# Optimization experiments

Measured on AMD Instinct MI355X. Metric: run time of the kernel, lower is better.

## Reference

```python
import jax, jax.numpy as jnp
import numpy as np

RES = 64
FDIM = 32
NMOD = 3
HID = 64
NCLS = 4
NFREQ = 6
IN_DIM = FDIM * NMOD + 3 * (2 * NFREQ + 1)  # 135


def trilinear_sample(grid, pts):
    """Torch F.grid_sample(mode='bilinear', padding_mode='zeros', align_corners=True).
    grid: [C, D, H, W]; pts: [M, 3] with (x, y, z) in [-1, 1], x indexes W, y->H, z->D.
    Returns [M, C]."""
    C, D, H, W = grid.shape
    x, y, z = pts[:, 0], pts[:, 1], pts[:, 2]
    ix = (x + 1.0) * 0.5 * (W - 1)
    iy = (y + 1.0) * 0.5 * (H - 1)
    iz = (z + 1.0) * 0.5 * (D - 1)
    ix0 = jnp.floor(ix); iy0 = jnp.floor(iy); iz0 = jnp.floor(iz)
    fx = ix - ix0; fy = iy - iy0; fz = iz - iz0
    ix0i = ix0.astype(jnp.int32); ix1i = ix0i + 1
    iy0i = iy0.astype(jnp.int32); iy1i = iy0i + 1
    iz0i = iz0.astype(jnp.int32); iz1i = iz0i + 1

    def corner(zc, yc, xc, w):
        valid = ((zc >= 0) & (zc < D) & (yc >= 0) & (yc < H) & (xc >= 0) & (xc < W))
        zcc = jnp.clip(zc, 0, D - 1)
        ycc = jnp.clip(yc, 0, H - 1)
        xcc = jnp.clip(xc, 0, W - 1)
        v = grid[:, zcc, ycc, xcc]  # [C, M]
        return v * (w * valid.astype(grid.dtype))

    wx0 = 1.0 - fx; wx1 = fx
    wy0 = 1.0 - fy; wy1 = fy
    wz0 = 1.0 - fz; wz1 = fz
    out = (corner(iz0i, iy0i, ix0i, wz0 * wy0 * wx0)
           + corner(iz0i, iy0i, ix1i, wz0 * wy0 * wx1)
           + corner(iz0i, iy1i, ix0i, wz0 * wy1 * wx0)
           + corner(iz0i, iy1i, ix1i, wz0 * wy1 * wx1)
           + corner(iz1i, iy0i, ix0i, wz1 * wy0 * wx0)
           + corner(iz1i, iy0i, ix1i, wz1 * wy0 * wx1)
           + corner(iz1i, iy1i, ix0i, wz1 * wy1 * wx0)
           + corner(iz1i, iy1i, ix1i, wz1 * wy1 * wx1))
    return out.T  # [M, C]


def positional_encoding(x):
    # gamma(p) = [p, sin(2^0 pi p), cos(2^0 pi p), ..., sin(2^(L-1) pi p), cos(2^(L-1) pi p)]
    freqs = 2.0 ** jnp.arange(NFREQ, dtype=x.dtype)  # [L]
    enc = [x]
    for i in range(NFREQ):
        a = jnp.pi * freqs[i] * x
        enc.append(jnp.sin(a))
        enc.append(jnp.cos(a))
    return jnp.concatenate(enc, axis=-1)  # [..., 3*(2L+1)]


def setup_inputs() -> dict:
    key = jax.random.key(0)
    ks = jax.random.split(key, 8)
    B, N = 4, 131072
    points = jax.random.uniform(ks[0], (B, N, 3), jnp.float32, -1.0, 1.0)
    grids = jax.random.normal(ks[1], (NMOD, FDIM, RES, RES, RES), jnp.float32) * 0.1

    def xavier(k, fan_in, fan_out):
        a = np.sqrt(6.0 / (fan_in + fan_out))
        return jax.random.uniform(k, (fan_in, fan_out), jnp.float32, -a, a)

    W0 = xavier(ks[2], IN_DIM, HID); b0 = jnp.zeros((HID,), jnp.float32)
    W1 = xavier(ks[3], HID, HID); b1 = jnp.zeros((HID,), jnp.float32)
    W2 = xavier(ks[4], HID, 1 + NCLS); b2 = jnp.zeros((1 + NCLS,), jnp.float32)
    return {"points": points, "grids": grids, "W0": W0, "b0": b0,
            "W1": W1, "b1": b1, "W2": W2, "b2": b2}


def reference(points, grids, W0, b0, W1, b1, W2, b2):
    B, N, _ = points.shape
    pts = points.reshape(B * N, 3)
    # fuse all 3 modalities: cat along feature dim, modality-major order
    feats = jax.vmap(lambda g: trilinear_sample(g, pts))(grids)  # [3, M, C]
    fused = jnp.transpose(feats, (1, 0, 2)).reshape(B * N, NMOD * FDIM)
    pe = positional_encoding(pts)  # [M, 39]
    h = jnp.concatenate([fused, pe], axis=-1)  # [M, 135]
    h = jax.nn.relu(h @ W0 + b0)
    h = jax.nn.relu(h @ W1 + b1)
    o = h @ W2 + b2  # [M, 1 + num_classes]
    density = jax.nn.softplus(o[..., 0]).reshape(B, N)
    seg_logits = o[..., 1:].reshape(B, N, NCLS)
    return density, seg_logits
```

## Files before the change

kernel.cpp:

```cpp
#include <hip/hip_runtime.h>
#include <hip/hip_bf16.h>
#include <hip/hip_fp16.h>
#include <math.h>

#define RESX 64
#define NVOX (RESX * RESX * RESX)
#define FDIM 32
#define NMOD 3
#define HID 64
#define NCLS 4
#define NFREQ 6
#define INDIM 135
#define TPB 64
#define XK 168
#define XSTR 65
#define MSTRIDE_B (NVOX * FDIM * 2)
#define NCELL 4096
#define NREP 16
#define TRB (NMOD * (NVOX / 64))
#define HISTB 2048
#define PACKB 15

typedef _Float16 f16x8 __attribute__((ext_vector_type(8)));
typedef float    f32x4 __attribute__((ext_vector_type(4)));

static __device__ __forceinline__ __half2 u2h(unsigned int u) {
    return __builtin_bit_cast(__half2, u);
}
static __device__ __forceinline__ unsigned int h2u(__half2 h) {
    return __builtin_bit_cast(unsigned int, h);
}

static __device__ __forceinline__ int cell_coords(float px, float py, float pz,
                                                  int& x0, int& y0, int& z0) {
    x0 = (int)floorf((px + 1.0f) * 0.5f * (RESX - 1));
    y0 = (int)floorf((py + 1.0f) * 0.5f * (RESX - 1));
    z0 = (int)floorf((pz + 1.0f) * 0.5f * (RESX - 1));
    x0 = min(max(x0, 0), RESX - 1);
    y0 = min(max(y0, 0), RESX - 1);
    z0 = min(max(z0, 0), RESX - 1);
    return ((z0 >> 2) << 8) | ((y0 >> 2) << 4) | (x0 >> 2);
}

#define W0PACK (5 * 4 * 64 * 8)
#define W1PACK (2 * 4 * 64 * 8)
#define W2PACK (2 * 64 * 8)

__global__ void pre_kernel(const float* __restrict__ g,
                           _Float16* __restrict__ gt,
                           const float* __restrict__ W0,
                           const float* __restrict__ W1,
                           const float* __restrict__ W2,
                           _Float16* __restrict__ wb,
                           const float* __restrict__ points,
                           unsigned int* __restrict__ hist, int M) {
    __shared__ float tile[FDIM][65];
    const int bid = blockIdx.x;
    const int t   = threadIdx.x;
    if (bid < TRB) {
        const int m  = bid >> 12;
        const int v0 = (bid & 4095) << 6;
#pragma unroll
        for (int pass = 0; pass < 8; ++pass) {
            const int c = pass * 4 + (t >> 6);
            const int v = t & 63;
            tile[c][v] = g[(size_t)(m * FDIM + c) * NVOX + v0 + v];
        }
        __syncthreads();
        unsigned int* gtu = reinterpret_cast<unsigned int*>(gt);
#pragma unroll
        for (int pass = 0; pass < 4; ++pass) {
            const int flat = pass * 256 + t;
            const int v  = flat >> 4;
            const int cu = flat & 15;
            gtu[(size_t)(m * NVOX + v0 + v) * 16 + cu] =
                h2u(__floats2half2_rn(tile[2 * cu][v], tile[2 * cu + 1][v]));
        }
    } else if (bid < TRB + HISTB) {
        const int hb = bid - TRB;
        const int i  = hb * 256 + t;
        const int r  = hb & (NREP - 1);
        if (i < M) {
            int x0, y0, z0;
            const int c = cell_coords(points[i * 3], points[i * 3 + 1], points[i * 3 + 2],
                                      x0, y0, z0);
            atomicAdd(&hist[r * NCELL + c], 1u);
        }
    } else {
        const int tt = (bid - TRB - HISTB) * 256 + t;
        const int NT = PACKB * 256;
        for (int idx = tt; idx < W0PACK; idx += NT) {
            const int j = idx & 7, l = (idx >> 3) & 63, nt = (idx >> 9) & 3, s = idx >> 11;
            const int k = 32 * s + (l >> 4) * 8 + j;
            const int o = 16 * nt + (l & 15);
            wb[idx] = (_Float16)((k < INDIM) ? W0[k * HID + o] : 0.0f);
        }
        for (int idx = tt; idx < W1PACK; idx += NT) {
            const int j = idx & 7, l = (idx >> 3) & 63, nt = (idx >> 9) & 3, s = idx >> 11;
            const int k = 32 * s + (l >> 4) * 8 + j;
            const int o = 16 * nt + (l & 15);
            wb[W0PACK + idx] = (_Float16)W1[k * HID + o];
        }
        for (int idx = tt; idx < W2PACK; idx += NT) {
            const int j = idx & 7, l = (idx >> 3) & 63, s = idx >> 9;
            const int k = 32 * s + (l >> 4) * 8 + j;
            const int o = l & 15;
            wb[W0PACK + W1PACK + idx] =
                (_Float16)((o < NCLS + 1) ? W2[k * (NCLS + 1) + o] : 0.0f);
        }
    }
}

__global__ __launch_bounds__(1024) void scan_fuse_kernel(unsigned int* __restrict__ hist) {
    __shared__ unsigned int s[1024];
    const int t = threadIdx.x;
    unsigned int tot[4];
#pragma unroll
    for (int j = 0; j < 4; ++j) {
        const int c = 4 * t + j;
        unsigned int run = 0;
#pragma unroll
        for (int r = 0; r < NREP; ++r) {
            const unsigned int v = hist[r * NCELL + c];
            hist[r * NCELL + c] = run;
            run += v;
        }
        tot[j] = run;
    }
    const unsigned int sum = tot[0] + tot[1] + tot[2] + tot[3];
    s[t] = sum;
    __syncthreads();
    for (int off = 1; off < 1024; off <<= 1) {
        const unsigned int x = (t >= off) ? s[t - off] : 0u;
        __syncthreads();
        s[t] += x;
        __syncthreads();
    }
    unsigned int cb = s[t] - sum;
#pragma unroll
    for (int j = 0; j < 4; ++j) {
        const int c = 4 * t + j;
#pragma unroll
        for (int r = 0; r < NREP; ++r) hist[r * NCELL + c] += cb;
        cb += tot[j];
    }
}

__global__ void scatter_kernel(const float* __restrict__ points,
                               unsigned int* __restrict__ hist,
                               float4* __restrict__ pts4, int M) {
    const int i = blockIdx.x * 256 + threadIdx.x;
    if (i < M) {
        const float px = points[i * 3], py = points[i * 3 + 1], pz = points[i * 3 + 2];
        int x0, y0, z0;
        const int c = cell_coords(px, py, pz, x0, y0, z0);
        const int r = blockIdx.x & (NREP - 1);
        const unsigned int pos = atomicAdd(&hist[r * NCELL + c], 1u);
        pts4[pos] = make_float4(px, py, pz, __int_as_float(i));
    }
}

template <bool SORT>
__global__ __launch_bounds__(256, 6) void fused_mfma_kernel(
    const float* __restrict__ points,
    const float4* __restrict__ pts4,
    const _Float16* __restrict__ gt,
    const _Float16* __restrict__ wb,
    const float* __restrict__ b0, const float* __restrict__ b1,
    const float* __restrict__ b2,
    float* __restrict__ density, float* __restrict__ seg) {
    __shared__ __align__(16) _Float16 Xs[TPB * XK];
    __shared__ __align__(16) int4   PB[TPB];
    __shared__ __align__(16) float4 PW[TPB];
    __shared__ __align__(16) float4 PXI[TPB];
    __shared__ int PIdx[TPB];
    const int tid = threadIdx.x;
    const int chunk = gridDim.x >> 3;
    const int sbid  = (blockIdx.x & 7) * chunk + (blockIdx.x >> 3);
    const int p0    = sbid * TPB;

    const int l = tid & 63;
    const int w = __builtin_amdgcn_readfirstlane(tid >> 6);

    if (l < 16) {
        const int p  = w * 16 + l;
        const int sp = p0 + p;
        float px, py, pz; int gp;
        if (SORT) {
            const float4 q = pts4[sp];
            px = q.x; py = q.y; pz = q.z; gp = __float_as_int(q.w);
        } else {
            px = points[sp * 3]; py = points[sp * 3 + 1]; pz = points[sp * 3 + 2];
            gp = sp;
        }
        const float ix = (px + 1.0f) * 0.5f * (RESX - 1);
        const float iy = (py + 1.0f) * 0.5f * (RESX - 1);
        const float iz = (pz + 1.0f) * 0.5f * (RESX - 1);
        const float fx0 = floorf(ix), fy0 = floorf(iy), fz0 = floorf(iz);
        const float fx = ix - fx0, fy = iy - fy0, fz = iz - fz0;
        int x0 = (int)fx0, y0 = (int)fy0, z0 = (int)fz0;
        x0 = min(max(x0, 0), RESX - 1);
        y0 = min(max(y0, 0), RESX - 1);
        z0 = min(max(z0, 0), RESX - 1);
        const int y1 = min(y0 + 1, RESX - 1);
        const int z1 = min(z0 + 1, RESX - 1);
        const float wy0 = 1.0f - fy, wy1 = fy;
        const float wz0 = 1.0f - fz, wz1 = fz;
        PB[p] = make_int4((z0 * 4096 + y0 * 64 + x0) * 64,
                          (z0 * 4096 + y1 * 64 + x0) * 64,
                          (z1 * 4096 + y0 * 64 + x0) * 64,
                          (z1 * 4096 + y1 * 64 + x0) * 64);
        PW[p]  = make_float4(wz0 * wy0, wz0 * wy1, wz1 * wy0, wz1 * wy1);
        PXI[p] = make_float4(px, py, pz, fx);
        PIdx[p] = gp;
    }

    {
        const int hw   = tid >> 5;
        const int lane = tid & 31;
        const int half = lane >> 4;
        const int lc   = lane & 15;
        const char* gbase = reinterpret_cast<const char*>(gt) + lane * 4;
#pragma unroll
        for (int i = 0; i < 8; ++i) {
            const int p = hw * 8 + i;
            const int4   bq = PB[p];
            const float4 wq = PW[p];
            const float  fx = PXI[p].w;
            const float wxh = half ? fx : 1.0f - fx;
            const __half2 h00 = __float2half2_rn(wq.x * wxh);
            const __half2 h01 = __float2half2_rn(wq.y * wxh);
            const __half2 h10 = __float2half2_rn(wq.z * wxh);
            const __half2 h11 = __float2half2_rn(wq.w * wxh);
            unsigned int accu[NMOD];
#pragma unroll
            for (int m = 0; m < NMOD; ++m) {
                const char* gm = gbase + (size_t)m * MSTRIDE_B;
                const unsigned int u0 = *reinterpret_cast<const unsigned int*>(gm + bq.x);
                const unsigned int u1 = *reinterpret_cast<const unsigned int*>(gm + bq.y);
                const unsigned int u2 = *reinterpret_cast<const unsigned int*>(gm + bq.z);
                const unsigned int u3 = *reinterpret_cast<const unsigned int*>(gm + bq.w);
                __half2 a = __hmul2(h00, u2h(u0));
                a = __hfma2(h01, u2h(u1), a);
                a = __hfma2(h10, u2h(u2), a);
                a = __hfma2(h11, u2h(u3), a);
                accu[m] = h2u(a);
            }
#pragma unroll
            for (int m = 0; m < NMOD; ++m) {
                const unsigned int other = __shfl_xor(accu[m], 16, 64);
                const __half2 sum = __hadd2(u2h(accu[m]), u2h(other));
                if (lane < 16) {
                    *reinterpret_cast<unsigned int*>(&Xs[p * XK + m * FDIM + 2 * lc]) = h2u(sum);
                }
            }
        }
    }

    {
        const int pt  = w * 16 + (l & 15);
        const int gq2 = l >> 4;
        const float4 pxi = PXI[pt];
        const float c3[3] = {pxi.x, pxi.y, pxi.z};
        _Float16* xr = &Xs[pt * XK];
        if (gq2 == 3) {
            xr[96]  = (_Float16)c3[0];
            xr[97]  = (_Float16)c3[1];
            xr[98]  = (_Float16)c3[2];
            xr[135] = (_Float16)0.0f;
        }
        if (gq2 == 2) {
            unsigned int* xz = reinterpret_cast<unsigned int*>(&xr[136]);
#pragma unroll
            for (int k = 0; k < 12; ++k) xz[k] = 0u;
        }
        {
            const int f = gq2;
            const float hf = 0.5f * (float)(1 << f);
#pragma unroll
            for (int d = 0; d < 3; ++d) {
                const float r  = c3[d] * hf;
                const float rf = r - floorf(r);
                xr[99 + 6 * f + d]     = (_Float16)__builtin_amdgcn_sinf(rf);
                xr[99 + 6 * f + 3 + d] = (_Float16)__builtin_amdgcn_cosf(rf);
            }
        }
        if (gq2 < 2) {
            const int f = gq2 + 4;
            const float hf = 0.5f * (float)(1 << f);
#pragma unroll
            for (int d = 0; d < 3; ++d) {
                const float r  = c3[d] * hf;
                const float rf = r - floorf(r);
                xr[99 + 6 * f + d]     = (_Float16)__builtin_amdgcn_sinf(rf);
                xr[99 + 6 * f + 3 + d] = (_Float16)__builtin_amdgcn_cosf(rf);
            }
        }
    }

    const int col = l & 15;
    const int g   = l >> 4;

    f32x4 acc0[4];
#pragma unroll
    for (int nt = 0; nt < 4; ++nt) {
        const float bv = b0[nt * 16 + col];
        acc0[nt] = (f32x4){bv, bv, bv, bv};
    }
    {
        const _Float16* arow = &Xs[(w * 16 + col) * XK];
#pragma unroll
        for (int s = 0; s < 5; ++s) {
            const f16x8 af = *reinterpret_cast<const f16x8*>(arow + s * 32 + g * 8);
#pragma unroll
            for (int nt = 0; nt < 4; ++nt) {
                const f16x8 bfr = *reinterpret_cast<const f16x8*>(wb + (size_t)((s * 4 + nt) * 64 + l) * 8);
                acc0[nt] = __builtin_amdgcn_mfma_f32_16x16x32_f16(af, bfr, acc0[nt], 0, 0, 0);
            }
        }
    }
#pragma unroll
    for (int nt = 0; nt < 4; ++nt)
#pragma unroll
        for (int r = 0; r < 4; ++r) {
            Xs[(w * 16 + g * 4 + r) * XK + 96 + nt * 16 + col] =
                (_Float16)fmaxf(acc0[nt][r], 0.0f);
        }

    f32x4 acc1[4];
#pragma unroll
    for (int nt = 0; nt < 4; ++nt) {
        const float bv = b1[nt * 16 + col];
        acc1[nt] = (f32x4){bv, bv, bv, bv};
    }
    {
        const _Float16* arow = &Xs[(w * 16 + col) * XK + 96];
        const _Float16* wb1  = wb + W0PACK;
#pragma unroll
        for (int s = 0; s < 2; ++s) {
            const f16x8 af = *reinterpret_cast<const f16x8*>(arow + s * 32 + g * 8);
#pragma unroll
            for (int nt = 0; nt < 4; ++nt) {
                const f16x8 bfr = *reinterpret_cast<const f16x8*>(wb1 + (size_t)((s * 4 + nt) * 64 + l) * 8);
                acc1[nt] = __builtin_amdgcn_mfma_f32_16x16x32_f16(af, bfr, acc1[nt], 0, 0, 0);
            }
        }
    }
#pragma unroll
    for (int nt = 0; nt < 4; ++nt)
#pragma unroll
        for (int r = 0; r < 4; ++r) {
            Xs[(w * 16 + g * 4 + r) * XK + nt * 16 + col] =
                (_Float16)fmaxf(acc1[nt][r], 0.0f);
        }

    f32x4 acc2;
    {
        const float bv = (col < NCLS + 1) ? b2[col] : 0.0f;
        acc2 = (f32x4){bv, bv, bv, bv};
        const _Float16* arow = &Xs[(w * 16 + col) * XK];
        const _Float16* wb2  = wb + W0PACK + W1PACK;
#pragma unroll
        for (int s = 0; s < 2; ++s) {
            const f16x8 af  = *reinterpret_cast<const f16x8*>(arow + s * 32 + g * 8);
            const f16x8 bfr = *reinterpret_cast<const f16x8*>(wb2 + (size_t)(s * 64 + l) * 8);
            acc2 = __builtin_amdgcn_mfma_f32_16x16x32_f16(af, bfr, acc2, 0, 0, 0);
        }
    }
    if (col < NCLS + 1) {
        float* osr = reinterpret_cast<float*>(&Xs[0]);
#pragma unroll
        for (int r = 0; r < 4; ++r) {
            const int row = w * 16 + g * 4 + r;
            osr[(row * XK + 128) / 2 + col] = acc2[r];
        }
    }

    if (l < 16) {
        const int row = w * 16 + l;
        const int gp2 = PIdx[row];
        const float* osr = reinterpret_cast<const float*>(&Xs[0]) + (row * XK + 128) / 2;
        const float4 o0123 = *reinterpret_cast<const float4*>(osr);
        const float o4 = osr[4];
        const float e  = __builtin_amdgcn_exp2f(fabsf(o0123.x) * -1.44269504f);
        const float sp = fmaxf(o0123.x, 0.0f) + 0.69314718f * __builtin_amdgcn_logf(1.0f + e);
        density[gp2] = sp;
        reinterpret_cast<float4*>(seg)[gp2] = make_float4(o0123.y, o0123.z, o0123.w, o4);
    }
}

__global__ __launch_bounds__(256, 4) void fused_nerf_fallback(
    const float* __restrict__ points,
    const float* __restrict__ grids,
    const float* __restrict__ W0, const float* __restrict__ b0,
    const float* __restrict__ W1, const float* __restrict__ b1,
    const float* __restrict__ W2, const float* __restrict__ b2,
    float* __restrict__ density, float* __restrict__ seg) {
    __shared__ float xT[INDIM + 1][XSTR];
    const int tid = threadIdx.x;
    const int p0  = blockIdx.x * TPB;
    {
        const int hw   = tid >> 5;
        const int lane = tid & 31;
        for (int i = 0; i < TPB / 8; ++i) {
            const int p  = hw * (TPB / 8) + i;
            const int gp = p0 + p;
            const float px = points[gp * 3 + 0];
            const float py = points[gp * 3 + 1];
            const float pz = points[gp * 3 + 2];
            const float ix = (px + 1.0f) * 0.5f * (RESX - 1);
            const float iy = (py + 1.0f) * 0.5f * (RESX - 1);
            const float iz = (pz + 1.0f) * 0.5f * (RESX - 1);
            const float fx0 = floorf(ix), fy0 = floorf(iy), fz0 = floorf(iz);
            const float fx = ix - fx0, fy = iy - fy0, fz = iz - fz0;
            int ix0 = (int)fx0, iy0 = (int)fy0, iz0 = (int)fz0;
            ix0 = min(max(ix0, 0), RESX - 1);
            iy0 = min(max(iy0, 0), RESX - 1);
            iz0 = min(max(iz0, 0), RESX - 1);
            const int ix1 = min(ix0 + 1, RESX - 1);
            const int iy1 = min(iy0 + 1, RESX - 1);
            const int iz1 = min(iz0 + 1, RESX - 1);
            const float wx1 = fx, wx0 = 1.0f - fx;
            const float wy1 = fy, wy0 = 1.0f - fy;
            const float wz1 = fz, wz0 = 1.0f - fz;
            const int vz0 = iz0 * 4096, vz1 = iz1 * 4096;
            const int vy0 = iy0 * 64,   vy1 = iy1 * 64;
            const int v000 = vz0 + vy0 + ix0, v001 = vz0 + vy0 + ix1;
            const int v010 = vz0 + vy1 + ix0, v011 = vz0 + vy1 + ix1;
            const int v100 = vz1 + vy0 + ix0, v101 = vz1 + vy0 + ix1;
            const int v110 = vz1 + vy1 + ix0, v111 = vz1 + vy1 + ix1;
            const float w000 = wz0 * wy0 * wx0, w001 = wz0 * wy0 * wx1;
            const float w010 = wz0 * wy1 * wx0, w011 = wz0 * wy1 * wx1;
            const float w100 = wz1 * wy0 * wx0, w101 = wz1 * wy0 * wx1;
            const float w110 = wz1 * wy1 * wx0, w111 = wz1 * wy1 * wx1;
#pragma unroll
            for (int m = 0; m < NMOD; ++m) {
                const float* gb = grids + (size_t)(m * FDIM + lane) * NVOX;
                float acc;
                acc = w000 * gb[v000];
                acc = fmaf(w001, gb[v001], acc);
                acc = fmaf(w010, gb[v010], acc);
                acc = fmaf(w011, gb[v011], acc);
                acc = fmaf(w100, gb[v100], acc);
                acc = fmaf(w101, gb[v101], acc);
                acc = fmaf(w110, gb[v110], acc);
                acc = fmaf(w111, gb[v111], acc);
                xT[m * FDIM + lane][p] = acc;
            }
        }
    }
    {
        const int p  = tid & 63;
        const int gq = tid >> 6;
        const int gp = p0 + p;
        float c3[3];
        c3[0] = points[gp * 3 + 0];
        c3[1] = points[gp * 3 + 1];
        c3[2] = points[gp * 3 + 2];
        if (gq == 3) {
#pragma unroll
            for (int d = 0; d < 3; ++d) xT[96 + d][p] = c3[d];
        }
#pragma unroll
        for (int f = 0; f < NFREQ; ++f) {
            if ((f & 3) != gq) continue;
            const float fr = (float)(1 << f);
#pragma unroll
            for (int d = 0; d < 3; ++d) {
                const float a = 3.14159274101257324f * fr * c3[d];
                xT[99 + 6 * f + d][p]     = sinf(a);
                xT[99 + 6 * f + 3 + d][p] = cosf(a);
            }
        }
    }
    __syncthreads();
    const int pl = tid & 63;
    const int wv = __builtin_amdgcn_readfirstlane(tid >> 6);
    const int gp = p0 + pl;
    float acc[16];
#pragma unroll
    for (int j = 0; j < 16; ++j) acc[j] = b0[wv * 16 + j];
    for (int k = 0; k < INDIM; ++k) {
        const float xk = xT[k][pl];
        const float* wr = W0 + k * HID + wv * 16;
#pragma unroll
        for (int j = 0; j < 16; ++j) acc[j] = fmaf(xk, wr[j], acc[j]);
    }
#pragma unroll
    for (int j = 0; j < 16; ++j) acc[j] = fmaxf(acc[j], 0.0f);
    __syncthreads();
#pragma unroll
    for (int j = 0; j < 16; ++j) xT[wv * 16 + j][pl] = acc[j];
    __syncthreads();
    float acc1[16];
#pragma unroll
    for (int j = 0; j < 16; ++j) acc1[j] = b1[wv * 16 + j];
    for (int k = 0; k < HID; ++k) {
        const float xk = xT[k][pl];
        const float* wr = W1 + k * HID + wv * 16;
#pragma unroll
        for (int j = 0; j < 16; ++j) acc1[j] = fmaf(xk, wr[j], acc1[j]);
    }
#pragma unroll
    for (int j = 0; j < 16; ++j) acc1[j] = fmaxf(acc1[j], 0.0f);
    __syncthreads();
#pragma unroll
    for (int j = 0; j < 16; ++j) xT[wv * 16 + j][pl] = acc1[j];
    __syncthreads();
    if (wv == 0) {
        float o[5];
#pragma unroll
        for (int j = 0; j < 5; ++j) o[j] = b2[j];
        for (int k = 0; k < HID; ++k) {
            const float xk = xT[k][pl];
            const float* wr = W2 + k * (1 + NCLS);
#pragma unroll
            for (int j = 0; j < 5; ++j) o[j] = fmaf(xk, wr[j], o[j]);
        }
        const float d = fmaxf(o[0], 0.0f) + log1pf(expf(-fabsf(o[0])));
        density[gp] = d;
        reinterpret_cast<float4*>(seg)[gp] = make_float4(o[1], o[2], o[3], o[4]);
    }
}

extern "C" void kernel_launch(void* const* d_in, const int* in_sizes, int n_in,
                              void* d_out, int out_size, void* d_ws, size_t ws_size,
                              hipStream_t stream) {
    const float* points = (const float*)d_in[0];
    const float* grids  = (const float*)d_in[1];
    const float* W0     = (const float*)d_in[2];
    const float* b0     = (const float*)d_in[3];
    const float* W1     = (const float*)d_in[4];
    const float* b1     = (const float*)d_in[5];
    const float* W2     = (const float*)d_in[6];
    const float* b2     = (const float*)d_in[7];

    const int M = in_sizes[0] / 3;
    float* density = (float*)d_out;
    float* seg     = density + M;

    const size_t gt_b   = (size_t)NMOD * NVOX * FDIM * sizeof(_Float16);
    const size_t wb_b   = 32768;
    const size_t hist_b = (size_t)NREP * NCELL * sizeof(unsigned int);
    const size_t pts_b  = (size_t)M * sizeof(float4);
    const int nblk = M / TPB;

    if (ws_size >= gt_b + wb_b + hist_b + pts_b) {
        char* p = (char*)d_ws;
        _Float16*     gt   = (_Float16*)p;      p += gt_b;
        _Float16*     wbp  = (_Float16*)p;      p += wb_b;
        unsigned int* hist = (unsigned int*)p;  p += hist_b;
        float4*       pts4 = (float4*)p;

        hipMemsetAsync(hist, 0, hist_b, stream);
        pre_kernel<<<TRB + HISTB + PACKB, 256, 0, stream>>>(
            grids, gt, W0, W1, W2, wbp, points, hist, M);
        scan_fuse_kernel<<<1, 1024, 0, stream>>>(hist);
        scatter_kernel<<<(M + 255) / 256, 256, 0, stream>>>(points, hist, pts4, M);
        fused_mfma_kernel<true><<<nblk, 256, 0, stream>>>(
            points, pts4, gt, wbp, b0, b1, b2, density, seg);
    } else if (ws_size >= gt_b + wb_b) {
        char* p = (char*)d_ws;
        _Float16* gt  = (_Float16*)p;  p += gt_b;
        _Float16* wbp = (_Float16*)p;
        pre_kernel<<<TRB + HISTB + PACKB, 256, 0, stream>>>(
            grids, gt, W0, W1, W2, wbp, points, (unsigned int*)nullptr, 0);
        fused_mfma_kernel<false><<<nblk, 256, 0, stream>>>(
            points, (const float4*)nullptr, gt, wbp, b0, b1, b2, density, seg);
    } else {
        fused_nerf_fallback<<<nblk, 256, 0, stream>>>(
            points, grids, W0, b0, W1, b1, W2, b2, density, seg);
    }
}
```

Measured before the change: 155.8 us.

## Store feature grid in 4x4x4 bricked layout and shrink per-point shared metadata

Rewrites the fp16 grid transpose so that voxels are stored in 4x4x4 bricks matching the sort cells, and computes gather addresses via a tiled index with a per-point x+1 delta, so that neighbouring-voxel reads stay within nearby cache lines. Per-point weights are now packed as half2 in LDS together with fx and the delta, and point coordinates and indices are kept in registers and passed with shuffles instead of being staged in shared memory. This cuts LDS footprint and instruction count, and the launch-bounds occupancy hint is raised from 6 to 7. Computing the weight products in half precision adds some rounding.

```diff
diff --git a/kernel.cpp b/kernel.cpp
--- a/kernel.cpp
+++ b/kernel.cpp
@@ -31,6 +31,12 @@
     return __builtin_bit_cast(unsigned int, h);
 }
 
+static __device__ __forceinline__ int tiled_byte(int x, int y, int z) {
+    const int cell = ((z >> 2) << 8) | ((y >> 2) << 4) | (x >> 2);
+    const int loc  = ((z & 3) << 4) | ((y & 3) << 2) | (x & 3);
+    return (cell * 64 + loc) * 64;
+}
+
 static __device__ __forceinline__ int cell_coords(float px, float py, float pz,
                                                   int& x0, int& y0, int& z0) {
     x0 = (int)floorf((px + 1.0f) * 0.5f * (RESX - 1));
@@ -71,10 +77,13 @@
 #pragma unroll
         for (int pass = 0; pass < 4; ++pass) {
             const int flat = pass * 256 + t;
-            const int v  = flat >> 4;
+            const int vi = flat >> 4;
             const int cu = flat & 15;
-            gtu[(size_t)(m * NVOX + v0 + v) * 16 + cu] =
-                h2u(__floats2half2_rn(tile[2 * cu][v], tile[2 * cu + 1][v]));
+            const int v  = v0 + vi;
+            const int x = v & 63, y = (v >> 6) & 63, z = v >> 12;
+            const int tb = tiled_byte(x, y, z) >> 2;
+            gtu[(size_t)m * (MSTRIDE_B / 4) + tb + cu] =
+                h2u(__floats2half2_rn(tile[2 * cu][vi], tile[2 * cu + 1][vi]));
         }
     } else if (bid < TRB + HISTB) {
         const int hb = bid - TRB;
@@ -161,7 +170,7 @@
 }
 
 template <bool SORT>
-__global__ __launch_bounds__(256, 6) void fused_mfma_kernel(
+__global__ __launch_bounds__(256, 7) void fused_mfma_kernel(
     const float* __restrict__ points,
     const float4* __restrict__ pts4,
     const _Float16* __restrict__ gt,
@@ -170,10 +179,9 @@
     const float* __restrict__ b2,
     float* __restrict__ density, float* __restrict__ seg) {
     __shared__ __align__(16) _Float16 Xs[TPB * XK];
-    __shared__ __align__(16) int4   PB[TPB];
-    __shared__ __align__(16) float4 PW[TPB];
-    __shared__ __align__(16) float4 PXI[TPB];
-    __shared__ int PIdx[TPB];
+    __shared__ __align__(16) int4  PB[TPB];
+    __shared__ __align__(8)  uint2 PWh[TPB];
+    __shared__ unsigned int FD[TPB];
     const int tid = threadIdx.x;
     const int chunk = gridDim.x >> 3;
     const int sbid  = (blockIdx.x & 7) * chunk + (blockIdx.x >> 3);
@@ -182,10 +190,11 @@
     const int l = tid & 63;
     const int w = __builtin_amdgcn_readfirstlane(tid >> 6);
 
+    float px = 0.0f, py = 0.0f, pz = 0.0f;
+    int gp = 0;
     if (l < 16) {
         const int p  = w * 16 + l;
         const int sp = p0 + p;
-        float px, py, pz; int gp;
         if (SORT) {
             const float4 q = pts4[sp];
             px = q.x; py = q.y; pz = q.z; gp = __float_as_int(q.w);
@@ -206,13 +215,13 @@
         const int z1 = min(z0 + 1, RESX - 1);
         const float wy0 = 1.0f - fy, wy1 = fy;
         const float wz0 = 1.0f - fz, wz1 = fz;
-        PB[p] = make_int4((z0 * 4096 + y0 * 64 + x0) * 64,
-                          (z0 * 4096 + y1 * 64 + x0) * 64,
-                          (z1 * 4096 + y0 * 64 + x0) * 64,
-                          (z1 * 4096 + y1 * 64 + x0) * 64);
-        PW[p]  = make_float4(wz0 * wy0, wz0 * wy1, wz1 * wy0, wz1 * wy1);
-        PXI[p] = make_float4(px, py, pz, fx);
-        PIdx[p] = gp;
+        PB[p] = make_int4(tiled_byte(x0, y0, z0), tiled_byte(x0, y1, z0),
+                          tiled_byte(x0, y0, z1), tiled_byte(x0, y1, z1));
+        PWh[p] = make_uint2(h2u(__floats2half2_rn(wz0 * wy0, wz0 * wy1)),
+                            h2u(__floats2half2_rn(wz1 * wy0, wz1 * wy1)));
+        const unsigned int delta = (x0 == RESX - 1) ? 0u : (((x0 & 3) == 3) ? 3904u : 64u);
+        const __half fxh = __float2half(fx);
+        FD[p] = (unsigned int)__builtin_bit_cast(unsigned short, fxh) | (delta << 16);
     }
 
     {
@@ -220,22 +229,28 @@
         const int lane = tid & 31;
         const int half = lane >> 4;
         const int lc   = lane & 15;
-        const char* gbase = reinterpret_cast<const char*>(gt) + lane * 4;
+        const char* gbase = reinterpret_cast<const char*>(gt) + lc * 4;
+        const __half2 one2 = __float2half2_rn(1.0f);
 #pragma unroll
         for (int i = 0; i < 8; ++i) {
             const int p = hw * 8 + i;
-            const int4   bq = PB[p];
-            const float4 wq = PW[p];
-            const float  fx = PXI[p].w;
-            const float wxh = half ? fx : 1.0f - fx;
-            const __half2 h00 = __float2half2_rn(wq.x * wxh);
-            const __half2 h01 = __float2half2_rn(wq.y * wxh);
-            const __half2 h10 = __float2half2_rn(wq.z * wxh);
-            const __half2 h11 = __float2half2_rn(wq.w * wxh);
+            const int4  bq = PB[p];
+            const uint2 pw = PWh[p];
+            const unsigned int fd = FD[p];
+            const __half fxh = __builtin_bit_cast(__half, (unsigned short)(fd & 0xffffu));
+            const unsigned int offH = half ? (fd >> 16) : 0u;
+            const __half2 fx2  = __half2half2(fxh);
+            const __half2 wxh2 = half ? fx2 : __hsub2(one2, fx2);
+            const __half2 wab = u2h(pw.x);
+            const __half2 wcd = u2h(pw.y);
+            const __half2 h00 = __hmul2(__low2half2(wab),  wxh2);
+            const __half2 h01 = __hmul2(__high2half2(wab), wxh2);
+            const __half2 h10 = __hmul2(__low2half2(wcd),  wxh2);
+            const __half2 h11 = __hmul2(__high2half2(wcd), wxh2);
             unsigned int accu[NMOD];
 #pragma unroll
             for (int m = 0; m < NMOD; ++m) {
-                const char* gm = gbase + (size_t)m * MSTRIDE_B;
+                const char* gm = gbase + (size_t)m * MSTRIDE_B + offH;
                 const unsigned int u0 = *reinterpret_cast<const unsigned int*>(gm + bq.x);
                 const unsigned int u1 = *reinterpret_cast<const unsigned int*>(gm + bq.y);
                 const unsigned int u2 = *reinterpret_cast<const unsigned int*>(gm + bq.z);
@@ -258,10 +273,13 @@
     }
 
     {
-        const int pt  = w * 16 + (l & 15);
+        const int src = l & 15;
+        const float c0 = __shfl(px, src, 64);
+        const float c1 = __shfl(py, src, 64);
+        const float c2 = __shfl(pz, src, 64);
+        const int pt  = w * 16 + src;
         const int gq2 = l >> 4;
-        const float4 pxi = PXI[pt];
-        const float c3[3] = {pxi.x, pxi.y, pxi.z};
+        const float c3[3] = {c0, c1, c2};
         _Float16* xr = &Xs[pt * XK];
         if (gq2 == 3) {
             xr[96]  = (_Float16)c3[0];
@@ -378,14 +396,13 @@
 
     if (l < 16) {
         const int row = w * 16 + l;
-        const int gp2 = PIdx[row];
         const float* osr = reinterpret_cast<const float*>(&Xs[0]) + (row * XK + 128) / 2;
         const float4 o0123 = *reinterpret_cast<const float4*>(osr);
         const float o4 = osr[4];
         const float e  = __builtin_amdgcn_exp2f(fabsf(o0123.x) * -1.44269504f);
         const float sp = fmaxf(o0123.x, 0.0f) + 0.69314718f * __builtin_amdgcn_logf(1.0f + e);
-        density[gp2] = sp;
-        reinterpret_cast<float4*>(seg)[gp2] = make_float4(o0123.y, o0123.z, o0123.w, o4);
+        density[gp] = sp;
+        reinterpret_cast<float4*>(seg)[gp] = make_float4(o0123.y, o0123.z, o0123.w, o4);
     }
 }
 
```

After: 161.7 us. 3.8% more time.

## Vectorize grid transpose to fp16 and split histogram scan into parallel kernels

Applied to the files above, without the earlier changes.

The grid transpose now handles 128 voxels per block, reading float4 from global memory and writing 16-byte uint4 packed fp16 stores instead of 4-byte ones, so fewer and wider memory transactions are issued. The single-block scan, which serially walked 16 replicas for four cells per thread and then rewrote the whole histogram, is split in two: a multi-block replica scan and a small cell-base scan. Scatter then adds the per-cell base to the per-replica offset at use time. This adds one kernel launch and two small workspace buffers, and the float4 shared tile read pattern may cause bank conflicts.

```diff
diff --git a/kernel.cpp b/kernel.cpp
--- a/kernel.cpp
+++ b/kernel.cpp
@@ -17,7 +17,8 @@
 #define MSTRIDE_B (NVOX * FDIM * 2)
 #define NCELL 4096
 #define NREP 16
-#define TRB (NMOD * (NVOX / 64))
+#define NBT (NVOX / 128)
+#define TRB (NMOD * NBT)
 #define HISTB 2048
 #define PACKB 15
 
@@ -31,11 +32,10 @@
     return __builtin_bit_cast(unsigned int, h);
 }
 
-static __device__ __forceinline__ int cell_coords(float px, float py, float pz,
-                                                  int& x0, int& y0, int& z0) {
-    x0 = (int)floorf((px + 1.0f) * 0.5f * (RESX - 1));
-    y0 = (int)floorf((py + 1.0f) * 0.5f * (RESX - 1));
-    z0 = (int)floorf((pz + 1.0f) * 0.5f * (RESX - 1));
+static __device__ __forceinline__ int cell_of(float px, float py, float pz) {
+    int x0 = (int)floorf((px + 1.0f) * 0.5f * (RESX - 1));
+    int y0 = (int)floorf((py + 1.0f) * 0.5f * (RESX - 1));
+    int z0 = (int)floorf((pz + 1.0f) * 0.5f * (RESX - 1));
     x0 = min(max(x0, 0), RESX - 1);
     y0 = min(max(y0, 0), RESX - 1);
     z0 = min(max(z0, 0), RESX - 1);
@@ -54,36 +54,49 @@
                            _Float16* __restrict__ wb,
                            const float* __restrict__ points,
                            unsigned int* __restrict__ hist, int M) {
-    __shared__ float tile[FDIM][65];
+    __shared__ float4 tile4[FDIM][33];
     const int bid = blockIdx.x;
     const int t   = threadIdx.x;
     if (bid < TRB) {
-        const int m  = bid >> 12;
-        const int v0 = (bid & 4095) << 6;
-#pragma unroll
-        for (int pass = 0; pass < 8; ++pass) {
-            const int c = pass * 4 + (t >> 6);
-            const int v = t & 63;
-            tile[c][v] = g[(size_t)(m * FDIM + c) * NVOX + v0 + v];
+        const int m  = bid / NBT;
+        const int v0 = (bid % NBT) * 128;
+        const float4* g4 = reinterpret_cast<const float4*>(g);
+#pragma unroll
+        for (int k = 0; k < 4; ++k) {
+            const int idx = k * 256 + t;
+            const int c = idx >> 5, q = idx & 31;
+            tile4[c][q] = g4[((size_t)(m * FDIM + c) * NVOX + v0) / 4 + q];
         }
         __syncthreads();
-        unsigned int* gtu = reinterpret_cast<unsigned int*>(gt);
-#pragma unroll
-        for (int pass = 0; pass < 4; ++pass) {
-            const int flat = pass * 256 + t;
-            const int v  = flat >> 4;
-            const int cu = flat & 15;
-            gtu[(size_t)(m * NVOX + v0 + v) * 16 + cu] =
-                h2u(__floats2half2_rn(tile[2 * cu][v], tile[2 * cu + 1][v]));
+        uint4* gtu4 = reinterpret_cast<uint4*>(gt);
+#pragma unroll
+        for (int k = 0; k < 2; ++k) {
+            const int idx = k * 256 + t;
+            const int v = idx >> 2, q = idx & 3;
+            const int vq = v >> 2, vr = v & 3;
+            uint4 o;
+            {
+                const float a0 = reinterpret_cast<const float*>(&tile4[8 * q + 0][vq])[vr];
+                const float a1 = reinterpret_cast<const float*>(&tile4[8 * q + 1][vq])[vr];
+                const float a2 = reinterpret_cast<const float*>(&tile4[8 * q + 2][vq])[vr];
+                const float a3 = reinterpret_cast<const float*>(&tile4[8 * q + 3][vq])[vr];
+                const float a4 = reinterpret_cast<const float*>(&tile4[8 * q + 4][vq])[vr];
+                const float a5 = reinterpret_cast<const float*>(&tile4[8 * q + 5][vq])[vr];
+                const float a6 = reinterpret_cast<const float*>(&tile4[8 * q + 6][vq])[vr];
+                const float a7 = reinterpret_cast<const float*>(&tile4[8 * q + 7][vq])[vr];
+                o.x = h2u(__floats2half2_rn(a0, a1));
+                o.y = h2u(__floats2half2_rn(a2, a3));
+                o.z = h2u(__floats2half2_rn(a4, a5));
+                o.w = h2u(__floats2half2_rn(a6, a7));
+            }
+            gtu4[(size_t)(m * NVOX + v0 + v) * 4 + q] = o;
         }
     } else if (bid < TRB + HISTB) {
         const int hb = bid - TRB;
         const int i  = hb * 256 + t;
         const int r  = hb & (NREP - 1);
         if (i < M) {
-            int x0, y0, z0;
-            const int c = cell_coords(points[i * 3], points[i * 3 + 1], points[i * 3 + 2],
-                                      x0, y0, z0);
+            const int c = cell_of(points[i * 3], points[i * 3 + 1], points[i * 3 + 2]);
             atomicAdd(&hist[r * NCELL + c], 1u);
         }
     } else {
@@ -111,23 +124,27 @@
     }
 }
 
-__global__ __launch_bounds__(1024) void scan_fuse_kernel(unsigned int* __restrict__ hist) {
+__global__ void scan_rep_kernel(unsigned int* __restrict__ hist,
+                                unsigned int* __restrict__ tot) {
+    const int c = blockIdx.x * 256 + threadIdx.x;
+    unsigned int run = 0;
+#pragma unroll
+    for (int r = 0; r < NREP; ++r) {
+        const unsigned int v = hist[r * NCELL + c];
+        hist[r * NCELL + c] = run;
+        run += v;
+    }
+    tot[c] = run;
+}
+
+__global__ __launch_bounds__(1024) void scan_kernel(const unsigned int* __restrict__ tot,
+                                                    unsigned int* __restrict__ cbase) {
     __shared__ unsigned int s[1024];
     const int t = threadIdx.x;
-    unsigned int tot[4];
-#pragma unroll
-    for (int j = 0; j < 4; ++j) {
-        const int c = 4 * t + j;
-        unsigned int run = 0;
-#pragma unroll
-        for (int r = 0; r < NREP; ++r) {
-            const unsigned int v = hist[r * NCELL + c];
-            hist[r * NCELL + c] = run;
-            run += v;
-        }
-        tot[j] = run;
-    }
-    const unsigned int sum = tot[0] + tot[1] + tot[2] + tot[3];
+    unsigned int v[4];
+#pragma unroll
+    for (int j = 0; j < 4; ++j) v[j] = tot[4 * t + j];
+    const unsigned int sum = v[0] + v[1] + v[2] + v[3];
     s[t] = sum;
     __syncthreads();
     for (int off = 1; off < 1024; off <<= 1) {
@@ -136,26 +153,21 @@
         s[t] += x;
         __syncthreads();
     }
-    unsigned int cb = s[t] - sum;
-#pragma unroll
-    for (int j = 0; j < 4; ++j) {
-        const int c = 4 * t + j;
-#pragma unroll
-        for (int r = 0; r < NREP; ++r) hist[r * NCELL + c] += cb;
-        cb += tot[j];
-    }
+    unsigned int excl = s[t] - sum;
+#pragma unroll
+    for (int j = 0; j < 4; ++j) { cbase[4 * t + j] = excl; excl += v[j]; }
 }
 
 __global__ void scatter_kernel(const float* __restrict__ points,
+                               const unsigned int* __restrict__ cbase,
                                unsigned int* __restrict__ hist,
                                float4* __restrict__ pts4, int M) {
     const int i = blockIdx.x * 256 + threadIdx.x;
     if (i < M) {
         const float px = points[i * 3], py = points[i * 3 + 1], pz = points[i * 3 + 2];
-        int x0, y0, z0;
-        const int c = cell_coords(px, py, pz, x0, y0, z0);
+        const int c = cell_of(px, py, pz);
         const int r = blockIdx.x & (NREP - 1);
-        const unsigned int pos = atomicAdd(&hist[r * NCELL + c], 1u);
+        const unsigned int pos = cbase[c] + atomicAdd(&hist[r * NCELL + c], 1u);
         pts4[pos] = make_float4(px, py, pz, __int_as_float(i));
     }
 }
@@ -542,21 +554,26 @@
     const size_t gt_b   = (size_t)NMOD * NVOX * FDIM * sizeof(_Float16);
     const size_t wb_b   = 32768;
     const size_t hist_b = (size_t)NREP * NCELL * sizeof(unsigned int);
+    const size_t tot_b  = NCELL * sizeof(unsigned int);
+    const size_t cb_b   = NCELL * sizeof(unsigned int);
     const size_t pts_b  = (size_t)M * sizeof(float4);
     const int nblk = M / TPB;
 
-    if (ws_size >= gt_b + wb_b + hist_b + pts_b) {
+    if (ws_size >= gt_b + wb_b + hist_b + tot_b + cb_b + pts_b) {
         char* p = (char*)d_ws;
-        _Float16*     gt   = (_Float16*)p;      p += gt_b;
-        _Float16*     wbp  = (_Float16*)p;      p += wb_b;
-        unsigned int* hist = (unsigned int*)p;  p += hist_b;
-        float4*       pts4 = (float4*)p;
+        _Float16*     gt    = (_Float16*)p;      p += gt_b;
+        _Float16*     wbp   = (_Float16*)p;      p += wb_b;
+        unsigned int* hist  = (unsigned int*)p;  p += hist_b;
+        unsigned int* tot   = (unsigned int*)p;  p += tot_b;
+        unsigned int* cbase = (unsigned int*)p;  p += cb_b;
+        float4*       pts4  = (float4*)p;
 
         hipMemsetAsync(hist, 0, hist_b, stream);
         pre_kernel<<<TRB + HISTB + PACKB, 256, 0, stream>>>(
             grids, gt, W0, W1, W2, wbp, points, hist, M);
-        scan_fuse_kernel<<<1, 1024, 0, stream>>>(hist);
-        scatter_kernel<<<(M + 255) / 256, 256, 0, stream>>>(points, hist, pts4, M);
+        scan_rep_kernel<<<NCELL / 256, 256, 0, stream>>>(hist, tot);
+        scan_kernel<<<1, 1024, 0, stream>>>(tot, cbase);
+        scatter_kernel<<<(M + 255) / 256, 256, 0, stream>>>(points, cbase, hist, pts4, M);
         fused_mfma_kernel<true><<<nblk, 256, 0, stream>>>(
             points, pts4, gt, wbp, b0, b1, b2, density, seg);
     } else if (ws_size >= gt_b + wb_b) {
```

Result: faster. 150.0 us (-3.7%).
